# Optimization experiments

Measured on AMD Instinct MI355X. Metric: run time of the kernel, lower is better.

## Reference

```python
import jax, jax.numpy as jnp
import numpy as np

HEADS = 4


def setup_inputs() -> dict:
    key = jax.random.key(0)
    ks = jax.random.split(key, 6)
    b, c, d, h, w = 4, 512, 16, 16, 16
    x = jax.random.normal(ks[0], (b, c, d, h, w), dtype=jnp.float32)
    s = 0.02  # param init scale
    Wq = jax.random.normal(ks[1], (c, c), dtype=jnp.float32) * s
    Wk = jax.random.normal(ks[2], (c, c), dtype=jnp.float32) * s
    Wv = jax.random.normal(ks[3], (c, c), dtype=jnp.float32) * s
    Wproj = jax.random.normal(ks[4], (c, c), dtype=jnp.float32) * s
    bproj = jnp.zeros((c,), dtype=jnp.float32)
    return {"x": x, "Wq": Wq, "Wk": Wk, "Wv": Wv, "Wproj": Wproj, "bproj": bproj}


def reference(x, Wq, Wk, Wv, Wproj, bproj):
    b, c, d, h, w = x.shape
    N = d * h * w
    scale = (c // HEADS) ** -0.5  # module uses ch//heads for scale
    xf = x.reshape(b, c, N)  # (b, c, N)
    # 1x1 Conv1d == channel matmul
    q = jnp.einsum('oc,bcn->bon', Wq, xf)
    k = jnp.einsum('oc,bcn->bon', Wk, xf)
    v = jnp.einsum('oc,bcn->bon', Wv, xf)
    # Faithful to original (buggy) view: split SEQUENCE dim by heads -> (b, H, c, N//H)
    q = q.reshape(b, HEADS, c, N // HEADS)
    k = k.reshape(b, HEADS, c, N // HEADS)
    v = v.reshape(b, HEADS, c, N // HEADS)
    attn = jax.nn.softmax(jnp.einsum('bhqe,bhke->bhqk', q, k) * scale, axis=-1)
    out = jnp.einsum('bhqk,bhke->bhqe', attn, v)  # (b, H, c, N//H)
    out = jnp.swapaxes(out, 2, 3).reshape(b, c, N)  # matches transpose(2,3).view
    out = jnp.einsum('oc,bcn->bon', Wproj, out) + bproj[None, :, None]
    return out.reshape(b, c, d, h, w) + x
```

## Files before the change

kernel.cpp:

```cpp
#include <hip/hip_runtime.h>
#include <stdint.h>


typedef __attribute__((ext_vector_type(8))) short short8;
typedef __attribute__((ext_vector_type(4))) float f32x4;

typedef const __attribute__((address_space(1))) unsigned int* gas_ptr;
typedef __attribute__((address_space(3))) unsigned int* las_ptr;

#define ATTN_SCALE 0.08838834764831845f

__device__ __forceinline__ unsigned short f2bf(float f) {
    union { float f; unsigned int u; } c; c.f = f;
    unsigned int u = c.u;
    u += 0x7fffu + ((u >> 16) & 1u);
    return (unsigned short)(u >> 16);
}

__device__ __forceinline__ void gl_lds16(const void* g, void* l) {
    __builtin_amdgcn_global_load_lds((gas_ptr)(uintptr_t)g, (las_ptr)(uintptr_t)l,
                                     16, 0, 0);
}

template<int LDA, int LDB, int KDIM, bool PERMB = false>
__device__ __forceinline__ void mfma_core(
    const unsigned short* __restrict__ A,
    const unsigned short* __restrict__ B,
    int m0, int n0,
    unsigned short* __restrict__ sA, unsigned short* __restrict__ sB,
    f32x4 acc[4][4])
{
    const int tid  = threadIdx.x;
    const int lane = tid & 63, wave = tid >> 6;
    const int lr = lane >> 2, lc = lane & 3;
    const int lcs = lc ^ ((lr >> 1) & 3);
    const int wm = (wave & 1) * 64, wn = (wave >> 1) * 64;
    const int col = lane & 15, quad = lane >> 4;
    const int swz = (quad ^ ((col >> 1) & 3)) * 8;

    const unsigned short* ga = A + (size_t)(m0 + 32 * wave + lr) * LDA + lcs * 8;
    int rb0 = n0 + 32 * wave + lr;
    int rb1 = rb0 + 16;
    if (PERMB) {
        rb0 = 4 * (rb0 & 127) + (rb0 >> 7);
        rb1 = 4 * (rb1 & 127) + (rb1 >> 7);
    }
    const unsigned short* gb0 = B + (size_t)rb0 * LDB + lcs * 8;
    const unsigned short* gb1 = B + (size_t)rb1 * LDB + lcs * 8;

    const int wr0 = (32 * wave) * 32;
    const int wr1 = (32 * wave + 16) * 32;

    gl_lds16(ga,            sA + wr0);
    gl_lds16(ga + 16 * LDA, sA + wr1);
    gl_lds16(gb0,           sB + wr0);
    gl_lds16(gb1,           sB + wr1);

    constexpr int NK = KDIM / 32;
    for (int kk = 0; kk < NK; ++kk) {
        const int bo = (kk & 1) * 4096;
        if (kk + 1 < NK) {
            const int nb = ((kk + 1) & 1) * 4096;
            const int k0 = (kk + 1) * 32;
            gl_lds16(ga + k0,            sA + nb + wr0);
            gl_lds16(ga + k0 + 16 * LDA, sA + nb + wr1);
            gl_lds16(gb0 + k0,           sB + nb + wr0);
            gl_lds16(gb1 + k0,           sB + nb + wr1);
            asm volatile("s_waitcnt vmcnt(4)" ::: "memory");
        } else {
            asm volatile("s_waitcnt vmcnt(0)" ::: "memory");
        }
        __builtin_amdgcn_s_barrier();
        asm volatile("" ::: "memory");
        __builtin_amdgcn_sched_barrier(0);

        const unsigned short* bA = sA + bo;
        const unsigned short* bB = sB + bo;
        short8 af[4], bfv[4];
        #pragma unroll
        for (int i = 0; i < 4; ++i)
            af[i] = *(const short8*)&bA[(wm + i * 16 + col) * 32 + swz];
        #pragma unroll
        for (int j = 0; j < 4; ++j)
            bfv[j] = *(const short8*)&bB[(wn + j * 16 + col) * 32 + swz];
        #pragma unroll
        for (int i = 0; i < 4; ++i)
            #pragma unroll
            for (int j = 0; j < 4; ++j)
                acc[i][j] = __builtin_amdgcn_mfma_f32_16x16x32_bf16(
                    af[i], bfv[j], acc[i][j], 0, 0, 0);

        __builtin_amdgcn_s_barrier();
        asm volatile("" ::: "memory");
    }
}

__global__ __launch_bounds__(256)
void prep(const float* __restrict__ x,
          const float* __restrict__ Wq, const float* __restrict__ Wk,
          const float* __restrict__ Wv, const float* __restrict__ Wp,
          unsigned short* __restrict__ xT, unsigned short* __restrict__ Wb)
{
    if (blockIdx.z == 4) {
        const int idx = (blockIdx.y * 64 + blockIdx.x) * 256 + threadIdx.x;
        const int mat = idx >> 16;
        const int off = (idx & 65535) << 2;
        const float* src = (mat == 0 ? Wq : mat == 1 ? Wk : mat == 2 ? Wv : Wp) + off;
        const float4 f = *(const float4*)src;
        uint2 o;
        o.x = f2bf(f.x) | ((unsigned)f2bf(f.y) << 16);
        o.y = f2bf(f.z) | ((unsigned)f2bf(f.w) << 16);
        *(uint2*)&Wb[mat * 262144 + off] = o;
        return;
    }
    const int b = blockIdx.z;
    const int l = threadIdx.x & 63, w = threadIdx.x >> 6;
    const int n  = blockIdx.x * 64 + l;
    const int c0 = blockIdx.y * 32 + w * 8;
    const float* xp = x + (size_t)b * 2097152 + (size_t)c0 * 4096 + n;
    unsigned int p[4];
    #pragma unroll
    for (int j = 0; j < 4; ++j) {
        const unsigned short a  = f2bf(xp[(2 * j)     * 4096]);
        const unsigned short bb = f2bf(xp[(2 * j + 1) * 4096]);
        p[j] = a | ((unsigned)bb << 16);
    }
    uint4 v; v.x = p[0]; v.y = p[1]; v.z = p[2]; v.w = p[3];
    *(uint4*)&xT[(size_t)b * 2097152 + (size_t)n * 512 + c0] = v;
}

__global__ __launch_bounds__(256)
void gemm_qkv(const unsigned short* __restrict__ Wb,
              const unsigned short* __restrict__ xT,
              unsigned short* __restrict__ qb, unsigned short* __restrict__ kb,
              unsigned short* __restrict__ vT)
{
    __shared__ unsigned short sT[128 * 136];
    unsigned short* sA = sT;
    unsigned short* sB = sT + 8192;

    const int z = blockIdx.z, wsel = z >> 2, b = z & 3;
    const unsigned short* A = Wb + wsel * 262144;
    const unsigned short* B = xT + (size_t)b * 2097152;
    const int m0 = blockIdx.y * 128, n0 = blockIdx.x * 128;

    f32x4 z4 = {0.f, 0.f, 0.f, 0.f};
    f32x4 acc[4][4];
    #pragma unroll
    for (int i = 0; i < 4; ++i)
        #pragma unroll
        for (int j = 0; j < 4; ++j) acc[i][j] = z4;

    mfma_core<512, 512, 512>(A, B, m0, n0, sA, sB, acc);

    __syncthreads();

    const int tid = threadIdx.x;
    const int lane = tid & 63, wave = tid >> 6;
    const int wm = (wave & 1) * 64, wn = (wave >> 1) * 64;
    const int col = lane & 15, quad = lane >> 4;
    const int h = m0 >> 7, s = n0 >> 10;

    if (wsel < 2) {
        #pragma unroll
        for (int i = 0; i < 4; ++i)
            #pragma unroll
            for (int r = 0; r < 4; ++r) {
                const int rr = wm + i * 16 + quad * 4 + r;
                #pragma unroll
                for (int j = 0; j < 4; ++j)
                    sT[rr * 136 + wn + j * 16 + col] = f2bf(acc[i][j][r]);
            }
        __syncthreads();
        unsigned short* C = (wsel == 0 ? qb : kb)
                          + (size_t)(b * 4 + h) * 524288;
        const int bKc = (n0 & 1023) >> 5;
        const int u = tid & 15, v = (tid >> 4) & 3, wv = tid >> 6;
        unsigned short* dst = C + (size_t)(s * 256 + bKc + wv) * 512
                            + (v * 16 + u) * 8;
        const unsigned short* src = sT + u * 136 + wv * 32 + v * 8;
        #pragma unroll
        for (int k = 0; k < 8; ++k)
            *(uint4*)(dst + k * 16384) = *(const uint4*)(src + k * 2176);
    } else {
        #pragma unroll
        for (int i = 0; i < 4; ++i)
            #pragma unroll
            for (int r = 0; r < 4; ++r) {
                const int rr = wm + i * 16 + quad * 4 + r;
                #pragma unroll
                for (int j = 0; j < 4; ++j)
                    sT[(wn + j * 16 + col) * 136 + rr] = f2bf(acc[i][j][r]);
            }
        __syncthreads();
        const int e0 = n0 & 1023;
        unsigned short* dst = vT + (size_t)(b * 4 + h) * 524288 + s * 128;
        const int u = tid & 15, rsel = tid >> 4;
        #pragma unroll
        for (int k = 0; k < 8; ++k) {
            const int ee = rsel + k * 16;
            *(uint4*)&dst[(size_t)(e0 + ee) * 512 + u * 8] =
                *(const uint4*)&sT[ee * 136 + u * 8];
        }
    }
}

__global__ __launch_bounds__(512)
void gemm_qks(const unsigned short* __restrict__ qb,
              const unsigned short* __restrict__ kb,
              unsigned short* __restrict__ P)
{
    __shared__ float red[2][32][8];
    const int d = blockIdx.x;
    const int flat = (d & 7) * 32 + (d >> 3);
    const int rg = flat & 15, z = flat >> 4;
    const unsigned short* Aq = qb + (size_t)z * 524288;
    const unsigned short* Bk = kb + (size_t)z * 524288;
    unsigned short* Pz = P + (size_t)z * 262144;

    const int tid = threadIdx.x;
    const int lane = tid & 63, w = tid >> 6;
    const int col = lane & 15, quad = lane >> 4;

    const unsigned short* ap0 = Aq + (size_t)((rg * 2 + 0) * 32) * 512 + lane * 8;
    const unsigned short* ap1 = Aq + (size_t)((rg * 2 + 1) * 32) * 512 + lane * 8;
    const unsigned short* bp0 = Bk + (size_t)((w * 4 + 0) * 32) * 512 + lane * 8;
    const unsigned short* bp1 = bp0 + 16384;
    const unsigned short* bp2 = bp0 + 32768;
    const unsigned short* bp3 = bp0 + 49152;

    f32x4 z4 = {0.f, 0.f, 0.f, 0.f};
    f32x4 acc[2][4];
    #pragma unroll
    for (int f = 0; f < 2; ++f)
        #pragma unroll
        for (int g = 0; g < 4; ++g) acc[f][g] = z4;

    #pragma unroll 4
    for (int kk = 0; kk < 32; ++kk) {
        const int o = kk * 512;
        const short8 af0 = *(const short8*)(ap0 + o);
        const short8 af1 = *(const short8*)(ap1 + o);
        short8 bf[4];
        bf[0] = *(const short8*)(bp0 + o);
        bf[1] = *(const short8*)(bp1 + o);
        bf[2] = *(const short8*)(bp2 + o);
        bf[3] = *(const short8*)(bp3 + o);
        #pragma unroll
        for (int g = 0; g < 4; ++g)
            acc[0][g] = __builtin_amdgcn_mfma_f32_16x16x32_bf16(
                af0, bf[g], acc[0][g], 0, 0, 0);
        #pragma unroll
        for (int g = 0; g < 4; ++g)
            acc[1][g] = __builtin_amdgcn_mfma_f32_16x16x32_bf16(
                af1, bf[g], acc[1][g], 0, 0, 0);
    }

    float mx[2][4];
    #pragma unroll
    for (int f = 0; f < 2; ++f)
        #pragma unroll
        for (int r = 0; r < 4; ++r) {
            float m = acc[f][0][r];
            #pragma unroll
            for (int g = 1; g < 4; ++g) m = fmaxf(m, acc[f][g][r]);
            #pragma unroll
            for (int s = 1; s < 16; s <<= 1) m = fmaxf(m, __shfl_xor(m, s));
            mx[f][r] = m;
        }
    if (col == 0) {
        #pragma unroll
        for (int f = 0; f < 2; ++f)
            #pragma unroll
            for (int r = 0; r < 4; ++r)
                red[0][f * 16 + quad * 4 + r][w] = mx[f][r];
    }
    __syncthreads();
    float sm[2][4];
    #pragma unroll
    for (int f = 0; f < 2; ++f)
        #pragma unroll
        for (int r = 0; r < 4; ++r) {
            const int row = f * 16 + quad * 4 + r;
            float m = red[0][row][0];
            #pragma unroll
            for (int t = 1; t < 8; ++t) m = fmaxf(m, red[0][row][t]);
            float s = 0.f;
            #pragma unroll
            for (int g = 0; g < 4; ++g) {
                const float e = __expf((acc[f][g][r] - m) * ATTN_SCALE);
                acc[f][g][r] = e;
                s += e;
            }
            #pragma unroll
            for (int t = 1; t < 16; t <<= 1) s += __shfl_xor(s, t);
            sm[f][r] = s;
        }
    if (col == 0) {
        #pragma unroll
        for (int f = 0; f < 2; ++f)
            #pragma unroll
            for (int r = 0; r < 4; ++r)
                red[1][f * 16 + quad * 4 + r][w] = sm[f][r];
    }
    __syncthreads();
    #pragma unroll
    for (int f = 0; f < 2; ++f)
        #pragma unroll
        for (int r = 0; r < 4; ++r) {
            const int row = f * 16 + quad * 4 + r;
            float tot = red[1][row][0];
            #pragma unroll
            for (int t = 1; t < 8; ++t) tot += red[1][row][t];
            const float inv = 1.f / tot;
            unsigned short* op = Pz + (size_t)(rg * 32 + row) * 512
                               + w * 64 + col;
            #pragma unroll
            for (int g = 0; g < 4; ++g)
                op[g * 16] = f2bf(acc[f][g][r] * inv);
        }
}

__global__ __launch_bounds__(256)
void gemm_pv(const unsigned short* __restrict__ Pb,
             const unsigned short* __restrict__ vT,
             unsigned short* __restrict__ yT)
{
    __shared__ unsigned short sT[128 * 136];
    unsigned short* sA = sT;
    unsigned short* sB = sT + 8192;
    const int z = blockIdx.z, b = z >> 2, hh = z & 3;
    const unsigned short* A = Pb + (size_t)z * 262144;
    const unsigned short* B = vT + (size_t)z * 524288;
    unsigned short* yTb = yT + (size_t)b * 2097152;
    const int m0 = blockIdx.y * 128;
    const int n0 = blockIdx.x * 128;

    f32x4 z4 = {0.f, 0.f, 0.f, 0.f};
    f32x4 acc[4][4];
    #pragma unroll
    for (int i = 0; i < 4; ++i)
        #pragma unroll
        for (int j = 0; j < 4; ++j) acc[i][j] = z4;

    mfma_core<512, 512, 512>(A, B, m0, n0, sA, sB, acc);

    __syncthreads();

    const int tid = threadIdx.x;
    const int lane = tid & 63, wave = tid >> 6;
    const int wm = (wave & 1) * 64, wn = (wave >> 1) * 64;
    const int col = lane & 15, quad = lane >> 4;

    #pragma unroll
    for (int i = 0; i < 4; ++i)
        #pragma unroll
        for (int r = 0; r < 4; ++r) {
            const int rr = wm + i * 16 + quad * 4 + r;
            #pragma unroll
            for (int j = 0; j < 4; ++j)
                sT[rr * 136 + wn + j * 16 + col] = f2bf(acc[i][j][r]);
        }
    __syncthreads();

    const int sblk = m0 >> 7;
    #pragma unroll
    for (int k = 0; k < 4; ++k) {
        const int rid = k * 256 + tid;
        const int qq_l = rid >> 3, s = rid & 7;
        const unsigned short* Trow = sT + qq_l * 136;
        unsigned int p[8];
        #pragma unroll
        for (int t = 0; t < 8; ++t) {
            const unsigned int a  = Trow[s + 8 * (2 * t)];
            const unsigned int bb = Trow[s + 8 * (2 * t + 1)];
            p[t] = a | (bb << 16);
        }
        const size_t base = (size_t)((s << 9) + 4 * qq_l + sblk) * 512
                          + hh * 128 + (n0 >> 3);
        uint4 lo; lo.x = p[0]; lo.y = p[1]; lo.z = p[2]; lo.w = p[3];
        uint4 hi; hi.x = p[4]; hi.y = p[5]; hi.z = p[6]; hi.w = p[7];
        *(uint4*)&yTb[base]     = lo;
        *(uint4*)&yTb[base + 8] = hi;
    }
}

__global__ __launch_bounds__(256)
void gemm_proj(const unsigned short* __restrict__ Wpb,
               const unsigned short* __restrict__ yT,
               const float* __restrict__ bias, const float* __restrict__ x,
               float* __restrict__ out)
{
    __shared__ unsigned short sA[2 * 128 * 32], sB[2 * 128 * 32];
    const int b = blockIdx.z;
    const unsigned short* B = yT + (size_t)b * 2097152;
    const int m0 = blockIdx.y * 128, n0 = blockIdx.x * 128;

    f32x4 z4 = {0.f, 0.f, 0.f, 0.f};
    f32x4 acc[4][4];
    #pragma unroll
    for (int i = 0; i < 4; ++i)
        #pragma unroll
        for (int j = 0; j < 4; ++j) acc[i][j] = z4;

    mfma_core<512, 512, 512>(Wpb, B, m0, n0, sA, sB, acc);

    const int lane = threadIdx.x & 63, wave = threadIdx.x >> 6;
    const int wm = (wave & 1) * 64, wn = (wave >> 1) * 64;
    const int col = lane & 15, quad = lane >> 4;
    const size_t boff = (size_t)b * 2097152;
    #pragma unroll
    for (int i = 0; i < 4; ++i)
        #pragma unroll
        for (int r = 0; r < 4; ++r) {
            const int row = m0 + wm + i * 16 + quad * 4 + r;
            const float bi = bias[row];
            #pragma unroll
            for (int j = 0; j < 4; ++j) {
                const size_t idx = boff + (size_t)row * 4096 + n0 + wn + j * 16 + col;
                out[idx] = acc[i][j][r] + bi + x[idx];
            }
        }
}

extern "C" void kernel_launch(void* const* d_in, const int* in_sizes, int n_in,
                              void* d_out, int out_size, void* d_ws, size_t ws_size,
                              hipStream_t stream) {
    const float* x     = (const float*)d_in[0];
    const float* Wq    = (const float*)d_in[1];
    const float* Wk    = (const float*)d_in[2];
    const float* Wv    = (const float*)d_in[3];
    const float* Wproj = (const float*)d_in[4];
    const float* bproj = (const float*)d_in[5];
    float* out = (float*)d_out;

    char* w = (char*)d_ws;
    unsigned short* xT = (unsigned short*)(w + 0);
    unsigned short* qb = (unsigned short*)(w + 16777216);
    unsigned short* kb = (unsigned short*)(w + 33554432);
    unsigned short* vT = (unsigned short*)(w + 50331648);
    unsigned short* Pb = (unsigned short*)(w + 100663296);
    unsigned short* Wb = (unsigned short*)(w + 109051904);
    unsigned short* yT = xT;

    prep        <<<dim3(64, 16, 5),  256, 0, stream>>>(x, Wq, Wk, Wv, Wproj, xT, Wb);
    gemm_qkv    <<<dim3(32, 4, 12),  256, 0, stream>>>(Wb, xT, qb, kb, vT);
    gemm_qks    <<<dim3(256),        512, 0, stream>>>(qb, kb, Pb);
    gemm_pv     <<<dim3(8, 4, 16),   256, 0, stream>>>(Pb, vT, yT);
    gemm_proj   <<<dim3(32, 4, 4),   256, 0, stream>>>(Wb + 3 * 262144, yT, bproj, x, out);
}
```

Measured before the change: 185.7 us.

## Remap GEMM block indices for XCD locality and split QK softmax across 16 waves

Remaps the flat block index in the qkv, pv and proj GEMMs so that blocks sharing the same operands land on the same XCD (a d&7 interleave), aiming to improve L2 reuse across the chiplets. The QK-softmax kernel now runs 1024 threads, with each wave computing one 16-row fragment instead of two. This doubles the waves available to hide global-load latency but halves per-wave reuse of the B fragments and raises register and occupancy pressure per block.

```diff
diff --git a/kernel.cpp b/kernel.cpp
--- a/kernel.cpp
+++ b/kernel.cpp
@@ -139,10 +139,14 @@
     unsigned short* sA = sT;
     unsigned short* sB = sT + 8192;
 
-    const int z = blockIdx.z, wsel = z >> 2, b = z & 3;
+    const int d = blockIdx.x + 32 * blockIdx.y + 128 * blockIdx.z;
+    const int f = (d & 7) * 192 + (d >> 3);
+    const int g = f >> 7, q = f & 127;
+    const int wsel = g % 3, b = g / 3;
+    const int m0 = (q & 3) * 128, n0 = (q >> 2) * 128;
+
     const unsigned short* A = Wb + wsel * 262144;
     const unsigned short* B = xT + (size_t)b * 2097152;
-    const int m0 = blockIdx.y * 128, n0 = blockIdx.x * 128;
 
     f32x4 z4 = {0.f, 0.f, 0.f, 0.f};
     f32x4 acc[4][4];
@@ -205,7 +209,7 @@
     }
 }
 
-__global__ __launch_bounds__(512)
+__global__ __launch_bounds__(1024)
 void gemm_qks(const unsigned short* __restrict__ qb,
               const unsigned short* __restrict__ kb,
               unsigned short* __restrict__ P)
@@ -220,27 +224,24 @@
 
     const int tid = threadIdx.x;
     const int lane = tid & 63, w = tid >> 6;
+    const int rw = w >> 3, cw = w & 7;
     const int col = lane & 15, quad = lane >> 4;
 
-    const unsigned short* ap0 = Aq + (size_t)((rg * 2 + 0) * 32) * 512 + lane * 8;
-    const unsigned short* ap1 = Aq + (size_t)((rg * 2 + 1) * 32) * 512 + lane * 8;
-    const unsigned short* bp0 = Bk + (size_t)((w * 4 + 0) * 32) * 512 + lane * 8;
+    const unsigned short* ap  = Aq + (size_t)((rg * 2 + rw) * 32) * 512 + lane * 8;
+    const unsigned short* bp0 = Bk + (size_t)((cw * 4 + 0) * 32) * 512 + lane * 8;
     const unsigned short* bp1 = bp0 + 16384;
     const unsigned short* bp2 = bp0 + 32768;
     const unsigned short* bp3 = bp0 + 49152;
 
     f32x4 z4 = {0.f, 0.f, 0.f, 0.f};
-    f32x4 acc[2][4];
-    #pragma unroll
-    for (int f = 0; f < 2; ++f)
-        #pragma unroll
-        for (int g = 0; g < 4; ++g) acc[f][g] = z4;
+    f32x4 acc[4];
+    #pragma unroll
+    for (int g = 0; g < 4; ++g) acc[g] = z4;
 
     #pragma unroll 4
     for (int kk = 0; kk < 32; ++kk) {
         const int o = kk * 512;
-        const short8 af0 = *(const short8*)(ap0 + o);
-        const short8 af1 = *(const short8*)(ap1 + o);
+        const short8 af = *(const short8*)(ap + o);
         short8 bf[4];
         bf[0] = *(const short8*)(bp0 + o);
         bf[1] = *(const short8*)(bp1 + o);
@@ -248,77 +249,62 @@
         bf[3] = *(const short8*)(bp3 + o);
         #pragma unroll
         for (int g = 0; g < 4; ++g)
-            acc[0][g] = __builtin_amdgcn_mfma_f32_16x16x32_bf16(
-                af0, bf[g], acc[0][g], 0, 0, 0);
+            acc[g] = __builtin_amdgcn_mfma_f32_16x16x32_bf16(
+                af, bf[g], acc[g], 0, 0, 0);
+    }
+
+    float mx[4];
+    #pragma unroll
+    for (int r = 0; r < 4; ++r) {
+        float m = acc[0][r];
+        #pragma unroll
+        for (int g = 1; g < 4; ++g) m = fmaxf(m, acc[g][r]);
+        #pragma unroll
+        for (int s = 1; s < 16; s <<= 1) m = fmaxf(m, __shfl_xor(m, s));
+        mx[r] = m;
+    }
+    if (col == 0) {
+        #pragma unroll
+        for (int r = 0; r < 4; ++r)
+            red[0][rw * 16 + quad * 4 + r][cw] = mx[r];
+    }
+    __syncthreads();
+    float sm[4];
+    #pragma unroll
+    for (int r = 0; r < 4; ++r) {
+        const int row = rw * 16 + quad * 4 + r;
+        float m = red[0][row][0];
+        #pragma unroll
+        for (int t = 1; t < 8; ++t) m = fmaxf(m, red[0][row][t]);
+        float s = 0.f;
+        #pragma unroll
+        for (int g = 0; g < 4; ++g) {
+            const float e = __expf((acc[g][r] - m) * ATTN_SCALE);
+            acc[g][r] = e;
+            s += e;
+        }
+        #pragma unroll
+        for (int t = 1; t < 16; t <<= 1) s += __shfl_xor(s, t);
+        sm[r] = s;
+    }
+    if (col == 0) {
+        #pragma unroll
+        for (int r = 0; r < 4; ++r)
+            red[1][rw * 16 + quad * 4 + r][cw] = sm[r];
+    }
+    __syncthreads();
+    #pragma unroll
+    for (int r = 0; r < 4; ++r) {
+        const int row = rw * 16 + quad * 4 + r;
+        float tot = red[1][row][0];
+        #pragma unroll
+        for (int t = 1; t < 8; ++t) tot += red[1][row][t];
+        const float inv = 1.f / tot;
+        unsigned short* op = Pz + (size_t)(rg * 32 + row) * 512 + cw * 64 + col;
         #pragma unroll
         for (int g = 0; g < 4; ++g)
-            acc[1][g] = __builtin_amdgcn_mfma_f32_16x16x32_bf16(
-                af1, bf[g], acc[1][g], 0, 0, 0);
-    }
-
-    float mx[2][4];
-    #pragma unroll
-    for (int f = 0; f < 2; ++f)
-        #pragma unroll
-        for (int r = 0; r < 4; ++r) {
-            float m = acc[f][0][r];
-            #pragma unroll
-            for (int g = 1; g < 4; ++g) m = fmaxf(m, acc[f][g][r]);
-            #pragma unroll
-            for (int s = 1; s < 16; s <<= 1) m = fmaxf(m, __shfl_xor(m, s));
-            mx[f][r] = m;
-        }
-    if (col == 0) {
-        #pragma unroll
-        for (int f = 0; f < 2; ++f)
-            #pragma unroll
-            for (int r = 0; r < 4; ++r)
-                red[0][f * 16 + quad * 4 + r][w] = mx[f][r];
-    }
-    __syncthreads();
-    float sm[2][4];
-    #pragma unroll
-    for (int f = 0; f < 2; ++f)
-        #pragma unroll
-        for (int r = 0; r < 4; ++r) {
-            const int row = f * 16 + quad * 4 + r;
-            float m = red[0][row][0];
-            #pragma unroll
-            for (int t = 1; t < 8; ++t) m = fmaxf(m, red[0][row][t]);
-            float s = 0.f;
-            #pragma unroll
-            for (int g = 0; g < 4; ++g) {
-                const float e = __expf((acc[f][g][r] - m) * ATTN_SCALE);
-                acc[f][g][r] = e;
-                s += e;
-            }
-            #pragma unroll
-            for (int t = 1; t < 16; t <<= 1) s += __shfl_xor(s, t);
-            sm[f][r] = s;
-        }
-    if (col == 0) {
-        #pragma unroll
-        for (int f = 0; f < 2; ++f)
-            #pragma unroll
-            for (int r = 0; r < 4; ++r)
-                red[1][f * 16 + quad * 4 + r][w] = sm[f][r];
-    }
-    __syncthreads();
-    #pragma unroll
-    for (int f = 0; f < 2; ++f)
-        #pragma unroll
-        for (int r = 0; r < 4; ++r) {
-            const int row = f * 16 + quad * 4 + r;
-            float tot = red[1][row][0];
-            #pragma unroll
-            for (int t = 1; t < 8; ++t) tot += red[1][row][t];
-            const float inv = 1.f / tot;
-            unsigned short* op = Pz + (size_t)(rg * 32 + row) * 512
-                               + w * 64 + col;
-            #pragma unroll
-            for (int g = 0; g < 4; ++g)
-                op[g * 16] = f2bf(acc[f][g][r] * inv);
-        }
+            op[g * 16] = f2bf(acc[g][r] * inv);
+    }
 }
 
 __global__ __launch_bounds__(256)
@@ -329,12 +315,16 @@
     __shared__ unsigned short sT[128 * 136];
     unsigned short* sA = sT;
     unsigned short* sB = sT + 8192;
-    const int z = blockIdx.z, b = z >> 2, hh = z & 3;
+
+    const int d = blockIdx.x + 8 * blockIdx.y + 32 * blockIdx.z;
+    const int f = (d & 7) * 64 + (d >> 3);
+    const int n0 = (f & 7) * 128;
+    const int m0 = ((f >> 3) & 3) * 128;
+    const int z = f >> 5, b = z >> 2, hh = z & 3;
+
     const unsigned short* A = Pb + (size_t)z * 262144;
     const unsigned short* B = vT + (size_t)z * 524288;
     unsigned short* yTb = yT + (size_t)b * 2097152;
-    const int m0 = blockIdx.y * 128;
-    const int n0 = blockIdx.x * 128;
 
     f32x4 z4 = {0.f, 0.f, 0.f, 0.f};
     f32x4 acc[4][4];
@@ -392,9 +382,14 @@
                float* __restrict__ out)
 {
     __shared__ unsigned short sA[2 * 128 * 32], sB[2 * 128 * 32];
-    const int b = blockIdx.z;
+
+    const int d = blockIdx.x + 32 * blockIdx.y + 128 * blockIdx.z;
+    const int f = (d & 7) * 64 + (d >> 3);
+    const int n0 = (f & 31) * 128;
+    const int m0 = ((f >> 5) & 3) * 128;
+    const int b  = f >> 7;
+
     const unsigned short* B = yT + (size_t)b * 2097152;
-    const int m0 = blockIdx.y * 128, n0 = blockIdx.x * 128;
 
     f32x4 z4 = {0.f, 0.f, 0.f, 0.f};
     f32x4 acc[4][4];
@@ -445,7 +440,7 @@
 
     prep        <<<dim3(64, 16, 5),  256, 0, stream>>>(x, Wq, Wk, Wv, Wproj, xT, Wb);
     gemm_qkv    <<<dim3(32, 4, 12),  256, 0, stream>>>(Wb, xT, qb, kb, vT);
-    gemm_qks    <<<dim3(256),        512, 0, stream>>>(qb, kb, Pb);
+    gemm_qks    <<<dim3(256),        1024, 0, stream>>>(qb, kb, Pb);
     gemm_pv     <<<dim3(8, 4, 16),   256, 0, stream>>>(Pb, vT, yT);
     gemm_proj   <<<dim3(32, 4, 4),   256, 0, stream>>>(Wb + 3 * 262144, yT, bproj, x, out);
 }
```

Measured after the change: 202.4 us. 9.0% more time.

## Fuse softmax-QK and PV GEMMs into one attention kernel keeping P in LDS

Applied to the files above, without the earlier changes.

Merges the QK^T+softmax kernel and the P·V kernel into a single attention kernel. The normalized probability tile stays in shared memory and is multiplied directly against V, which is read straight from global memory in an MFMA-fragment-friendly layout that the QKV kernel now writes. This removes the global round-trip of P and one kernel launch. In exchange, V fragments are loaded from global memory without LDS staging, and each block's PV work is limited to 32 rows, which may lower MFMA efficiency or raise pressure on the memory system.

```diff
diff --git a/kernel.cpp b/kernel.cpp
--- a/kernel.cpp
+++ b/kernel.cpp
@@ -194,29 +194,34 @@
             }
         __syncthreads();
         const int e0 = n0 & 1023;
-        unsigned short* dst = vT + (size_t)(b * 4 + h) * 524288 + s * 128;
-        const int u = tid & 15, rsel = tid >> 4;
-        #pragma unroll
-        for (int k = 0; k < 8; ++k) {
-            const int ee = rsel + k * 16;
-            *(uint4*)&dst[(size_t)(e0 + ee) * 512 + u * 8] =
-                *(const uint4*)&sT[ee * 136 + u * 8];
-        }
+        unsigned short* dstb = vT + (size_t)(b * 4 + h) * 524288;
+        const int ce = tid & 15, j = tid >> 4;
+        const size_t base = (size_t)((e0 >> 4) * 32 + s * 4 + (j >> 2)) * 512
+                          + ((j & 3) * 16 + ce) * 8;
+        const unsigned short* srcb = sT + ce * 136 + j * 8;
+        #pragma unroll
+        for (int Re = 0; Re < 8; ++Re)
+            *(uint4*)&dstb[base + (size_t)Re * 16384]
+                = *(const uint4*)&srcb[Re * 2176];
     }
 }
 
 __global__ __launch_bounds__(512)
-void gemm_qks(const unsigned short* __restrict__ qb,
-              const unsigned short* __restrict__ kb,
-              unsigned short* __restrict__ P)
+void attn(const unsigned short* __restrict__ qb,
+          const unsigned short* __restrict__ kb,
+          const unsigned short* __restrict__ vTf,
+          unsigned short* __restrict__ yT)
 {
+    __shared__ unsigned short Pl[32 * 520];
     __shared__ float red[2][32][8];
     const int d = blockIdx.x;
     const int flat = (d & 7) * 32 + (d >> 3);
     const int rg = flat & 15, z = flat >> 4;
+    const int b = z >> 2, hh = z & 3;
     const unsigned short* Aq = qb + (size_t)z * 524288;
     const unsigned short* Bk = kb + (size_t)z * 524288;
-    unsigned short* Pz = P + (size_t)z * 262144;
+    const unsigned short* Vz = vTf + (size_t)z * 524288;
+    unsigned short* yTb = yT + (size_t)b * 2097152;
 
     const int tid = threadIdx.x;
     const int lane = tid & 63, w = tid >> 6;
@@ -313,75 +318,70 @@
             #pragma unroll
             for (int t = 1; t < 8; ++t) tot += red[1][row][t];
             const float inv = 1.f / tot;
-            unsigned short* op = Pz + (size_t)(rg * 32 + row) * 512
-                               + w * 64 + col;
             #pragma unroll
             for (int g = 0; g < 4; ++g)
-                op[g * 16] = f2bf(acc[f][g][r] * inv);
-        }
-}
-
-__global__ __launch_bounds__(256)
-void gemm_pv(const unsigned short* __restrict__ Pb,
-             const unsigned short* __restrict__ vT,
-             unsigned short* __restrict__ yT)
-{
-    __shared__ unsigned short sT[128 * 136];
-    unsigned short* sA = sT;
-    unsigned short* sB = sT + 8192;
-    const int z = blockIdx.z, b = z >> 2, hh = z & 3;
-    const unsigned short* A = Pb + (size_t)z * 262144;
-    const unsigned short* B = vT + (size_t)z * 524288;
-    unsigned short* yTb = yT + (size_t)b * 2097152;
-    const int m0 = blockIdx.y * 128;
-    const int n0 = blockIdx.x * 128;
-
-    f32x4 z4 = {0.f, 0.f, 0.f, 0.f};
-    f32x4 acc[4][4];
-    #pragma unroll
-    for (int i = 0; i < 4; ++i)
-        #pragma unroll
-        for (int j = 0; j < 4; ++j) acc[i][j] = z4;
-
-    mfma_core<512, 512, 512>(A, B, m0, n0, sA, sB, acc);
-
+                Pl[row * 520 + w * 64 + g * 16 + col] =
+                    f2bf(acc[f][g][r] * inv);
+        }
     __syncthreads();
 
-    const int tid = threadIdx.x;
-    const int lane = tid & 63, wave = tid >> 6;
-    const int wm = (wave & 1) * 64, wn = (wave >> 1) * 64;
-    const int col = lane & 15, quad = lane >> 4;
-
-    #pragma unroll
-    for (int i = 0; i < 4; ++i)
-        #pragma unroll
-        for (int r = 0; r < 4; ++r) {
-            const int rr = wm + i * 16 + quad * 4 + r;
-            #pragma unroll
-            for (int j = 0; j < 4; ++j)
-                sT[rr * 136 + wn + j * 16 + col] = f2bf(acc[i][j][r]);
-        }
+    f32x4 accp[2][8];
+    #pragma unroll
+    for (int f = 0; f < 2; ++f)
+        #pragma unroll
+        for (int g2 = 0; g2 < 8; ++g2) accp[f][g2] = z4;
+
+    #pragma unroll 2
+    for (int Kc = 0; Kc < 16; ++Kc) {
+        const short8 a0 = *(const short8*)&Pl[col * 520 + Kc * 32 + quad * 8];
+        const short8 a1 = *(const short8*)&Pl[(16 + col) * 520 + Kc * 32 + quad * 8];
+        short8 bv[8];
+        #pragma unroll
+        for (int g2 = 0; g2 < 8; ++g2)
+            bv[g2] = *(const short8*)&Vz[(size_t)((w * 8 + g2) * 32 + Kc) * 512
+                                         + lane * 8];
+        #pragma unroll
+        for (int g2 = 0; g2 < 8; ++g2) {
+            accp[0][g2] = __builtin_amdgcn_mfma_f32_16x16x32_bf16(
+                a0, bv[g2], accp[0][g2], 0, 0, 0);
+            accp[1][g2] = __builtin_amdgcn_mfma_f32_16x16x32_bf16(
+                a1, bv[g2], accp[1][g2], 0, 0, 0);
+        }
+    }
     __syncthreads();
 
-    const int sblk = m0 >> 7;
-    #pragma unroll
-    for (int k = 0; k < 4; ++k) {
-        const int rid = k * 256 + tid;
-        const int qq_l = rid >> 3, s = rid & 7;
-        const unsigned short* Trow = sT + qq_l * 136;
-        unsigned int p[8];
-        #pragma unroll
-        for (int t = 0; t < 8; ++t) {
-            const unsigned int a  = Trow[s + 8 * (2 * t)];
-            const unsigned int bb = Trow[s + 8 * (2 * t + 1)];
-            p[t] = a | (bb << 16);
-        }
-        const size_t base = (size_t)((s << 9) + 4 * qq_l + sblk) * 512
-                          + hh * 128 + (n0 >> 3);
-        uint4 lo; lo.x = p[0]; lo.y = p[1]; lo.z = p[2]; lo.w = p[3];
-        uint4 hi; hi.x = p[4]; hi.y = p[5]; hi.z = p[6]; hi.w = p[7];
-        *(uint4*)&yTb[base]     = lo;
-        *(uint4*)&yTb[base + 8] = hi;
+    unsigned short* Ol = Pl;
+    const int rl = tid >> 4, s8 = (tid >> 1) & 7, hw = tid & 1;
+    const int qsem = ((rg & 3) << 7) + 4 * rl + (rg >> 2);
+    const size_t nbase = (size_t)(s8 * 512 + qsem) * 512 + hh * 128;
+    #pragma unroll
+    for (int h2 = 0; h2 < 2; ++h2) {
+        if ((w >> 2) == h2) {
+            const int wl = w & 3;
+            #pragma unroll
+            for (int f = 0; f < 2; ++f)
+                #pragma unroll
+                for (int g2 = 0; g2 < 8; ++g2)
+                    #pragma unroll
+                    for (int r = 0; r < 4; ++r)
+                        Ol[(f * 16 + quad * 4 + r) * 520
+                           + wl * 128 + g2 * 16 + col] = f2bf(accp[f][g2][r]);
+        }
+        __syncthreads();
+        #pragma unroll
+        for (int v2 = 0; v2 < 4; ++v2) {
+            const int cdb = hw * 32 + v2 * 8;
+            unsigned int p[4];
+            #pragma unroll
+            for (int t = 0; t < 4; ++t) {
+                const unsigned int a  = Ol[rl * 520 + s8 + 8 * (cdb + 2 * t)];
+                const unsigned int bb = Ol[rl * 520 + s8 + 8 * (cdb + 2 * t + 1)];
+                p[t] = a | (bb << 16);
+            }
+            uint4 o; o.x = p[0]; o.y = p[1]; o.z = p[2]; o.w = p[3];
+            *(uint4*)&yTb[nbase + h2 * 64 + cdb] = o;
+        }
+        __syncthreads();
     }
 }
 
@@ -439,13 +439,11 @@
     unsigned short* qb = (unsigned short*)(w + 16777216);
     unsigned short* kb = (unsigned short*)(w + 33554432);
     unsigned short* vT = (unsigned short*)(w + 50331648);
-    unsigned short* Pb = (unsigned short*)(w + 100663296);
     unsigned short* Wb = (unsigned short*)(w + 109051904);
     unsigned short* yT = xT;
 
     prep        <<<dim3(64, 16, 5),  256, 0, stream>>>(x, Wq, Wk, Wv, Wproj, xT, Wb);
     gemm_qkv    <<<dim3(32, 4, 12),  256, 0, stream>>>(Wb, xT, qb, kb, vT);
-    gemm_qks    <<<dim3(256),        512, 0, stream>>>(qb, kb, Pb);
-    gemm_pv     <<<dim3(8, 4, 16),   256, 0, stream>>>(Pb, vT, yT);
+    attn        <<<dim3(256),        512, 0, stream>>>(qb, kb, vT, yT);
     gemm_proj   <<<dim3(32, 4, 4),   256, 0, stream>>>(Wb + 3 * 262144, yT, bproj, x, out);
 }
```

After: 192.6 us. +3.8%, slower.
